# Kernel tuning notes

Measured on AMD Instinct MI355X. Metric: run time of the kernel, lower is better.

The kernel has to match this reference:

```python
import jax, jax.numpy as jnp
import numpy as np

N_HEADS = 16
DIM = 1024
HW = 32
B = 8


def _conv3x3(x, W, b):
    # x: [B, C, H, W], W: [O, I, 3, 3] (OIHW), padding 1 == SAME for stride 1
    y = jax.lax.conv_general_dilated(
        x, W, window_strides=(1, 1), padding='SAME',
        dimension_numbers=('NCHW', 'OIHW', 'NCHW'))
    return y + b[None, :, None, None]


def setup_inputs() -> dict:
    key = jax.random.key(0)
    ks = jax.random.split(key, 8)
    f32 = jnp.float32
    q = jax.random.normal(ks[0], (B, DIM, HW, HW), f32)
    k = jax.random.normal(ks[1], (B, DIM, HW, HW), f32)
    v = jax.random.normal(ks[2], (B, DIM, HW, HW), f32)
    Wq = jax.random.normal(ks[3], (DIM, DIM, 3, 3), f32) * 0.02
    Wk = jax.random.normal(ks[4], (DIM, DIM, 3, 3), f32) * 0.02
    Wv = jax.random.normal(ks[5], (DIM, DIM, 3, 3), f32) * 0.02
    Wo = jax.random.normal(ks[6], (DIM, DIM), f32) * 0.02
    bq = jnp.zeros((DIM,), f32); bk = jnp.zeros((DIM,), f32)
    bv = jnp.zeros((DIM,), f32); bo = jnp.zeros((DIM,), f32)
    mask = jax.random.randint(ks[7], (B, DIM, DIM), 0, 2, jnp.int32)
    return {'q': q, 'k': k, 'v': v, 'Wq': Wq, 'bq': bq, 'Wk': Wk, 'bk': bk,
            'Wv': Wv, 'bv': bv, 'Wo': Wo, 'bo': bo, 'mask': mask}


def reference(q, k, v, Wq, bq, Wk, bk, Wv, bv, Wo, bo, mask):
    Bq, C, H, W = q.shape  # C == dim, tokens = channels
    h = N_HEADS
    d = (H * W) // h  # head dim

    def split_heads(x):
        # [B, C, H, W] -> [B, h, C, d]
        return x.reshape(Bq, C, h, d).transpose(0, 2, 1, 3)

    qh = split_heads(_conv3x3(q, Wq, bq))
    kh = split_heads(_conv3x3(k, Wk, bk))
    vh = split_heads(_conv3x3(v, Wv, bv))

    scale = 1.0 / np.sqrt(d).astype(np.float32)
    attn = jnp.einsum('bhtd,bhsd->bhts', qh, kh) * scale  # [B, h, C, C]
    attn = jnp.where(mask[:, None, :, :] == 0, jnp.float32(-1e9), attn)
    w = jax.nn.softmax(attn, axis=-1)  # attn_dropout rate = 0 -> identity
    out = jnp.einsum('bhts,bhsd->bhtd', w, vh)  # [B, h, C, d]
    out = out.transpose(0, 2, 1, 3).reshape(Bq, C, h * d)  # [B, C, H*W]
    out = out @ Wo.T + bo  # Linear(dim, dim); H*W == dim
    return out
```

## Files before the change

### kernel.cpp

```cpp
#include <hip/hip_runtime.h>

typedef __attribute__((ext_vector_type(8))) short bh8;
typedef __attribute__((ext_vector_type(4))) short bh4;
typedef __attribute__((ext_vector_type(4))) float f32x4;

__device__ __forceinline__ short f2bf(float f) {
  union { float f; unsigned u; } a; a.f = f;
  unsigned r = a.u + 0x7FFFu + ((a.u >> 16) & 1u);
  return (short)(r >> 16);
}

__device__ __forceinline__ void g2l16(const short* g, short* l) {
  __builtin_amdgcn_global_load_lds(
      (const __attribute__((address_space(1))) void*)g,
      (__attribute__((address_space(3))) void*)l, 16, 0, 0);
}

__device__ __forceinline__ void barrier_raw() {
  asm volatile("" ::: "memory");
  __builtin_amdgcn_s_barrier();
  asm volatile("" ::: "memory");
}

__global__ __launch_bounds__(256) void zero_halo(short* __restrict__ xP) {
  int z = blockIdx.y;
  short* base = xP + (size_t)z * 1183744;
  int ri = blockIdx.x * 2 + (threadIdx.x >> 7);
  int row;
  if (ri < 34) row = ri;
  else if (ri < 68) row = 1122 + (ri - 34);
  else { int j = ri - 68; int y = (j >> 1) + 1; int x = (j & 1) ? 33 : 0; row = y * 34 + x; }
  int col = (threadIdx.x & 127) * 8;
  bh8 zv = {0, 0, 0, 0, 0, 0, 0, 0};
  *(bh8*)(base + (size_t)row * 1024 + col) = zv;
}

__global__ __launch_bounds__(256) void transpose3(
    const float* __restrict__ q, const float* __restrict__ k, const float* __restrict__ v,
    short* __restrict__ qP, short* __restrict__ kP, short* __restrict__ vP) {
  int z = blockIdx.z; int tensor = z >> 3, b = z & 7;
  const float* src = tensor == 0 ? q : (tensor == 1 ? k : v);
  short* dst = tensor == 0 ? qP : (tensor == 1 ? kP : vP);
  src += (size_t)b * 1048576; dst += (size_t)b * 1183744;
  int row0 = blockIdx.y * 64;
  int col0 = blockIdx.x * 64;
  __shared__ short t[64][72];
  int tid = threadIdx.x;
#pragma unroll
  for (int i = 0; i < 2; ++i) {
    int cid = tid + i * 256;
    int r = cid >> 3, co = (cid & 7) * 8;
    const float* p = src + (size_t)(row0 + r) * 1024 + col0 + co;
    float4 f0 = *(const float4*)(p);
    float4 f1 = *(const float4*)(p + 4);
    t[co + 0][r] = f2bf(f0.x); t[co + 1][r] = f2bf(f0.y);
    t[co + 2][r] = f2bf(f0.z); t[co + 3][r] = f2bf(f0.w);
    t[co + 4][r] = f2bf(f1.x); t[co + 5][r] = f2bf(f1.y);
    t[co + 6][r] = f2bf(f1.z); t[co + 7][r] = f2bf(f1.w);
  }
  __syncthreads();
#pragma unroll
  for (int i = 0; i < 2; ++i) {
    int cid = tid + i * 256;
    int sr = cid >> 3, cc = (cid & 7) * 8;
    bh8 val = *(const bh8*)&t[sr][cc];
    int tok = col0 + sr;
    int pr = ((tok >> 5) + 1) * 34 + (tok & 31) + 1;
    *(bh8*)(dst + (size_t)pr * 1024 + row0 + cc) = val;
  }
}

__global__ __launch_bounds__(256) void wperm3(
    const float* __restrict__ Wq, const float* __restrict__ Wk, const float* __restrict__ Wv,
    short* __restrict__ WpQ, short* __restrict__ WpK, short* __restrict__ WpV) {
  int z = blockIdx.y;
  const float* W = z == 0 ? Wq : (z == 1 ? Wk : Wv);
  short* Wp = z == 0 ? WpQ : (z == 1 ? WpK : WpV);
  int idx = blockIdx.x * 256 + threadIdx.x;
  const float* wsrc = W + (size_t)idx * 9;
#pragma unroll
  for (int t = 0; t < 9; ++t) Wp[(size_t)t * 1048576 + idx] = f2bf(wsrc[t]);
}

__global__ __launch_bounds__(256) void cvt_bf(const float* __restrict__ src,
                                              short* __restrict__ dst) {
  int idx = (blockIdx.x * 256 + threadIdx.x) * 4;
  float4 f = *(const float4*)(src + idx);
  bh4 o; o[0] = f2bf(f.x); o[1] = f2bf(f.y); o[2] = f2bf(f.z); o[3] = f2bf(f.w);
  *(bh4*)(dst + idx) = o;
}

__global__ __launch_bounds__(256) void mask_pack(const int* __restrict__ m,
                                                 unsigned* __restrict__ mp) {
  int idx = blockIdx.x * 256 + threadIdx.x;
  const int* src = m + (size_t)idx * 32;
  unsigned wv = 0;
#pragma unroll
  for (int j = 0; j < 32; j += 4) {
    int4 a = *(const int4*)(src + j);
    wv |= ((unsigned)(a.x & 1) << j) | ((unsigned)(a.y & 1) << (j + 1)) |
          ((unsigned)(a.z & 1) << (j + 2)) | ((unsigned)(a.w & 1) << (j + 3));
  }
  mp[idx] = wv;
}

__global__ __launch_bounds__(256, 2) void conv_gemm_td(
    const short* __restrict__ WpQ, const short* __restrict__ WpK, const short* __restrict__ WpV,
    const short* __restrict__ xPq, const short* __restrict__ xPk, const short* __restrict__ xPv,
    short* __restrict__ cQ, short* __restrict__ cK, short* __restrict__ cVT,
    const float* __restrict__ bq, const float* __restrict__ bk, const float* __restrict__ bv,
    int convSel) {
  __shared__ short lds[36864];
  int tid = threadIdx.x, lane = tid & 63, wid = tid >> 6;

  int fid = blockIdx.x + (blockIdx.y << 2) + ((int)blockIdx.z << 5);
  int nwg = (int)gridDim.z << 5;
  int cpx = nwg >> 3;
  int swz = (fid & 7) * cpx + (fid >> 3);
  int mtile = swz & 3, ntile = (swz >> 2) & 7, z = swz >> 5;

  int conv = convSel >= 0 ? convSel : (z >> 3);
  int b = convSel >= 0 ? z : (z & 7);
  const short* Wp = conv == 0 ? WpQ : (conv == 1 ? WpK : WpV);
  const short* xP = conv == 0 ? xPq : (conv == 1 ? xPk : xPv);
  short* out = conv == 0 ? cQ : (conv == 1 ? cK : cVT);
  const float* bias = conv == 0 ? bq : (conv == 1 ? bk : bv);
  int XisA = (conv == 2);
  int mbase = mtile * 256, nbase = ntile * 128;
  const short* xb = xP + (size_t)b * 1183744;

  int srow = tid >> 2;
  int lsl = (tid & 3) ^ ((tid >> 3) & 3);
  int gcol = lsl * 8;
  const short* pA0; const short* pB0;
  ptrdiff_t jA, jB;
  if (!XisA) {
    pA0 = Wp + (size_t)(mbase + srow) * 1024 + gcol;
    jA = 65536;
    int tok = nbase + srow;
    pB0 = xb + (size_t)(((tok >> 5) + 1) * 34 + (tok & 31) + 1) * 1024 + gcol;
    jB = 69632;
  } else {
    int ta = mbase + srow;
    pA0 = xb + (size_t)(((ta >> 5) + 1) * 34 + (ta & 31) + 1) * 1024 + gcol;
    jA = 69632;
    pB0 = Wp + (size_t)(nbase + srow) * 1024 + gcol;
    jB = 65536;
  }
  int sdst = tid * 8;

  int pslot = (((lane >> 4) ^ ((lane >> 1) & 3)) << 3);
  int wr = wid >> 1, wc = wid & 1;
  int rdA = (wr * 128 + (lane & 15)) * 32 + pslot;
  int rdB = 8192 + (wc * 64 + (lane & 15)) * 32 + pslot;

  f32x4 acc[8][4] = {};

#define STAGE(U, SRB) do { \
    int u_ = (U); \
    int tap_ = u_ >> 5, kk_ = (u_ & 31) << 5; \
    int ty_ = (tap_ * 11) >> 5; \
    ptrdiff_t dW_ = (ptrdiff_t)tap_ * 1048576 + kk_; \
    ptrdiff_t dX_ = (ptrdiff_t)(ty_ * 34 + (tap_ - ty_ * 3) - 35) * 1024 + kk_; \
    ptrdiff_t dA_ = XisA ? dX_ : dW_, dB_ = XisA ? dW_ : dX_; \
    short* du_ = &lds[(SRB) + sdst]; \
    g2l16(pA0 + dA_,          du_); \
    g2l16(pA0 + dA_ + jA,     du_ + 2048); \
    g2l16(pA0 + dA_ + 2 * jA, du_ + 4096); \
    g2l16(pA0 + dA_ + 3 * jA, du_ + 6144); \
    g2l16(pB0 + dB_,          du_ + 8192); \
    g2l16(pB0 + dB_ + jB,     du_ + 10240); \
  } while (0)

  STAGE(0, 0);
  STAGE(1, 12288);
  asm volatile("s_waitcnt vmcnt(6)" ::: "memory");
  barrier_raw();

#define TILEBODY(RB, T, DOSTAGE, SRB, WSTR) do { \
    const short* Lp = &lds[(RB)]; \
    bh8 afr[4], bfr[4], afr2[4]; \
    _Pragma("unroll") for (int nt = 0; nt < 4; ++nt) \
      bfr[nt] = *(const bh8*)(Lp + rdB + nt * 512); \
    _Pragma("unroll") for (int mt = 0; mt < 4; ++mt) \
      afr[mt] = *(const bh8*)(Lp + rdA + mt * 512); \
    if (DOSTAGE) STAGE((T) + 2, SRB); \
    __builtin_amdgcn_s_setprio(1); \
    _Pragma("unroll") for (int mt = 0; mt < 4; ++mt) { \
      _Pragma("unroll") for (int nt = 0; nt < 4; ++nt) \
        acc[mt][nt] = __builtin_amdgcn_mfma_f32_16x16x32_bf16( \
            afr[mt], bfr[nt], acc[mt][nt], 0, 0, 0); \
    } \
    __builtin_amdgcn_s_setprio(0); \
    _Pragma("unroll") for (int mt = 0; mt < 4; ++mt) \
      afr2[mt] = *(const bh8*)(Lp + rdA + 2048 + mt * 512); \
    __builtin_amdgcn_s_setprio(1); \
    _Pragma("unroll") for (int mt = 0; mt < 4; ++mt) { \
      _Pragma("unroll") for (int nt = 0; nt < 4; ++nt) \
        acc[4 + mt][nt] = __builtin_amdgcn_mfma_f32_16x16x32_bf16( \
            afr2[mt], bfr[nt], acc[4 + mt][nt], 0, 0, 0); \
    } \
    __builtin_amdgcn_s_setprio(0); \
    asm volatile(WSTR ::: "memory"); \
    barrier_raw(); \
  } while (0)

#pragma unroll 1
  for (int it = 0; it < 95; ++it) {
    int t0 = it * 3;
    TILEBODY(0,     t0 + 0, true, 24576, "s_waitcnt vmcnt(6)");
    TILEBODY(12288, t0 + 1, true, 0,     "s_waitcnt vmcnt(6)");
    TILEBODY(24576, t0 + 2, true, 12288, "s_waitcnt vmcnt(6)");
  }
  TILEBODY(0,     285, true,  24576, "s_waitcnt vmcnt(6)");
  TILEBODY(12288, 286, false, 0,     "s_waitcnt vmcnt(0)");
  TILEBODY(24576, 287, false, 0,     "");

#undef TILEBODY
#undef STAGE

  size_t ob = (size_t)b * 1048576;
#pragma unroll
  for (int mt = 0; mt < 8; ++mt) {
#pragma unroll
    for (int nt = 0; nt < 4; ++nt) {
      int m0 = mbase + wr * 128 + mt * 16 + ((lane >> 4) << 2);
      int nn = nbase + wc * 64 + nt * 16 + (lane & 15);
#pragma unroll
      for (int r = 0; r < 4; ++r) {
        float bvv = bias[XisA ? nn : (m0 + r)];
        out[ob + (size_t)(m0 + r) * 1024 + nn] = f2bf(acc[mt][nt][r] + bvv);
      }
    }
  }
}

__global__ __launch_bounds__(256) void attn(
    const short* __restrict__ Qc, const short* __restrict__ Kc,
    const short* __restrict__ VT, const unsigned* __restrict__ Mp,
    short* __restrict__ AO) {
  __shared__ short sQ[64][72];
  __shared__ short sK[128][72];
  __shared__ short sV[64][136];
  __shared__ short sP[64][136];
  int tid = threadIdx.x, lane = tid & 63, w = tid >> 6;
  int qbase = blockIdx.x * 64, h = blockIdx.y, b = blockIdx.z;
  int j0 = h * 64;
  const short* Qb = Qc + (size_t)b * 1048576;
  const short* Kb = Kc + (size_t)b * 1048576;
  const short* Vb = VT + (size_t)b * 1048576;
  const unsigned* Mpb = Mp + (size_t)b * 32768;
  const float scale = 0.125f;

#pragma unroll
  for (int i = 0; i < 2; ++i) {
    int cid = tid + i * 256;
    int row = cid >> 3, co = (cid & 7) * 8;
    *(bh8*)&sQ[row][co] = *(const bh8*)(Qb + (size_t)(qbase + row) * 1024 + j0 + co);
  }
  __syncthreads();

  int tg = qbase + w * 16 + (lane & 15);
  int rsel = ((lane >> 4) << 2);
  float mrow = -3.0e38f, lrow = 0.0f;
  f32x4 oacc[4] = {};

  for (int st = 0; st < 8; ++st) {
#pragma unroll
    for (int i = 0; i < 4; ++i) {
      int cid = tid + i * 256;
      int row = cid >> 3, co = (cid & 7) * 8;
      *(bh8*)&sK[row][co] = *(const bh8*)(Kb + (size_t)(st * 128 + row) * 1024 + j0 + co);
      int vrow = cid >> 4, vco = (cid & 15) * 8;
      *(bh8*)&sV[vrow][vco] = *(const bh8*)(Vb + (size_t)(j0 + vrow) * 1024 + st * 128 + vco);
    }
    __syncthreads();

    f32x4 sacc[8];
#pragma unroll
    for (int mt = 0; mt < 8; ++mt) {
      f32x4 a = {0.f, 0.f, 0.f, 0.f};
      bh8 kf = *(const bh8*)&sK[mt * 16 + (lane & 15)][(lane >> 4) * 8];
      bh8 qf = *(const bh8*)&sQ[w * 16 + (lane & 15)][(lane >> 4) * 8];
      a = __builtin_amdgcn_mfma_f32_16x16x32_bf16(kf, qf, a, 0, 0, 0);
      kf = *(const bh8*)&sK[mt * 16 + (lane & 15)][32 + (lane >> 4) * 8];
      qf = *(const bh8*)&sQ[w * 16 + (lane & 15)][32 + (lane >> 4) * 8];
      a = __builtin_amdgcn_mfma_f32_16x16x32_bf16(kf, qf, a, 0, 0, 0);
      sacc[mt] = a;
    }

    uint4 Mw = *(const uint4*)(Mpb + (size_t)tg * 32 + st * 4);
    float tmax = -3.0e38f;
#pragma unroll
    for (int mt = 0; mt < 8; ++mt) {
      unsigned mwv = ((const unsigned*)&Mw)[mt >> 1] >> ((mt & 1) * 16 + rsel);
      f32x4 vv;
      vv[0] = (mwv & 1u) ? sacc[mt][0] * scale : -1e9f;
      vv[1] = (mwv & 2u) ? sacc[mt][1] * scale : -1e9f;
      vv[2] = (mwv & 4u) ? sacc[mt][2] * scale : -1e9f;
      vv[3] = (mwv & 8u) ? sacc[mt][3] * scale : -1e9f;
      sacc[mt] = vv;
      tmax = fmaxf(tmax, fmaxf(fmaxf(vv[0], vv[1]), fmaxf(vv[2], vv[3])));
    }
    tmax = fmaxf(tmax, __shfl_xor(tmax, 16, 64));
    tmax = fmaxf(tmax, __shfl_xor(tmax, 32, 64));
    float mnew = fmaxf(mrow, tmax);
    float alpha = __expf(fminf(mrow - mnew, 0.f));

    float sum = 0.f;
    uint4 Mw2 = Mw;
#pragma unroll
    for (int mt = 0; mt < 8; ++mt) {
      unsigned mwv = ((const unsigned*)&Mw2)[mt >> 1] >> ((mt & 1) * 16 + rsel);
      float p0 = (mwv & 1u) ? __expf(fminf(sacc[mt][0] - mnew, 0.f)) : 0.f;
      float p1 = (mwv & 2u) ? __expf(fminf(sacc[mt][1] - mnew, 0.f)) : 0.f;
      float p2 = (mwv & 4u) ? __expf(fminf(sacc[mt][2] - mnew, 0.f)) : 0.f;
      float p3 = (mwv & 8u) ? __expf(fminf(sacc[mt][3] - mnew, 0.f)) : 0.f;
      sum += (p0 + p1) + (p2 + p3);
      bh4 p; p[0] = f2bf(p0); p[1] = f2bf(p1); p[2] = f2bf(p2); p[3] = f2bf(p3);
      *(bh4*)&sP[w * 16 + (lane & 15)][mt * 16 + rsel] = p;
    }
    sum += __shfl_xor(sum, 16, 64);
    sum += __shfl_xor(sum, 32, 64);
    lrow = lrow * alpha + sum;
    mrow = mnew;

    float al[4];
#pragma unroll
    for (int r = 0; r < 4; ++r) al[r] = __shfl(alpha, rsel + r, 64);
#pragma unroll
    for (int nt = 0; nt < 4; ++nt)
#pragma unroll
      for (int r = 0; r < 4; ++r) oacc[nt][r] *= al[r];
    __syncthreads();

#pragma unroll
    for (int k0 = 0; k0 < 4; ++k0) {
      bh8 pf = *(const bh8*)&sP[w * 16 + (lane & 15)][k0 * 32 + (lane >> 4) * 8];
#pragma unroll
      for (int nt = 0; nt < 4; ++nt) {
        bh8 vf = *(const bh8*)&sV[nt * 16 + (lane & 15)][k0 * 32 + (lane >> 4) * 8];
        oacc[nt] = __builtin_amdgcn_mfma_f32_16x16x32_bf16(pf, vf, oacc[nt], 0, 0, 0);
      }
    }
    __syncthreads();
  }

  float rl[4];
#pragma unroll
  for (int r = 0; r < 4; ++r) rl[r] = 1.0f / __shfl(lrow, rsel + r, 64);
  size_t ob = (size_t)b * 1048576;
#pragma unroll
  for (int nt = 0; nt < 4; ++nt) {
    int j = nt * 16 + (lane & 15);
    int t0 = qbase + w * 16 + rsel;
#pragma unroll
    for (int r = 0; r < 4; ++r)
      AO[ob + (size_t)(t0 + r) * 1024 + j0 + j] = f2bf(oacc[nt][r] * rl[r]);
  }
}

__global__ __launch_bounds__(256) void gemm_bt(
    const short* __restrict__ A, const short* __restrict__ Bm,
    float* __restrict__ out, const float* __restrict__ bias) {
  __shared__ short sA[4096];
  __shared__ short sB[4096];
  int tid = threadIdx.x, lane = tid & 63, w = tid >> 6;
  int mbase = blockIdx.x * 128, nbase = blockIdx.y * 128;
  int colsh = (lane & 3) * 8;
  int ldsoff[2]; const short* ap[2]; const short* bp[2];
#pragma unroll
  for (int i = 0; i < 2; ++i) {
    int row = 32 * w + 16 * i + (lane >> 2);
    ldsoff[i] = (2 * w + i) * 512 + lane * 8;
    ap[i] = A + (size_t)(mbase + row) * 1024 + colsh;
    bp[i] = Bm + (size_t)(nbase + row) * 1024 + colsh;
  }
  f32x4 acc[4][4] = {};
  int wm = (w >> 1) * 64, wn = (w & 1) * 64;
  for (int kt = 0; kt < 1024; kt += 32) {
#pragma unroll
    for (int i = 0; i < 2; ++i) {
      g2l16(ap[i] + kt, sA + ldsoff[i]);
      g2l16(bp[i] + kt, sB + ldsoff[i]);
    }
    __syncthreads();
    bh8 af[4], bfr[4];
#pragma unroll
    for (int mt = 0; mt < 4; ++mt)
      af[mt] = *(const bh8*)&sA[(wm + mt * 16 + (lane & 15)) * 32 + (lane >> 4) * 8];
#pragma unroll
    for (int nt = 0; nt < 4; ++nt)
      bfr[nt] = *(const bh8*)&sB[(wn + nt * 16 + (lane & 15)) * 32 + (lane >> 4) * 8];
#pragma unroll
    for (int mt = 0; mt < 4; ++mt)
#pragma unroll
      for (int nt = 0; nt < 4; ++nt)
        acc[mt][nt] = __builtin_amdgcn_mfma_f32_16x16x32_bf16(af[mt], bfr[nt], acc[mt][nt], 0, 0, 0);
    __syncthreads();
  }
#pragma unroll
  for (int mt = 0; mt < 4; ++mt) {
#pragma unroll
    for (int nt = 0; nt < 4; ++nt) {
      int m0 = mbase + wm + mt * 16 + ((lane >> 4) << 2);
      int n = nbase + wn + nt * 16 + (lane & 15);
      float bv = bias[n];
#pragma unroll
      for (int r = 0; r < 4; ++r)
        out[(size_t)(m0 + r) * 1024 + n] = acc[mt][nt][r] + bv;
    }
  }
}

extern "C" void kernel_launch(void* const* d_in, const int* in_sizes, int n_in,
                              void* d_out, int out_size, void* d_ws, size_t ws_size,
                              hipStream_t stream) {
  (void)in_sizes; (void)n_in; (void)out_size;
  const float* q    = (const float*)d_in[0];
  const float* k    = (const float*)d_in[1];
  const float* v    = (const float*)d_in[2];
  const float* Wq   = (const float*)d_in[3];
  const float* bq   = (const float*)d_in[4];
  const float* Wk   = (const float*)d_in[5];
  const float* bk   = (const float*)d_in[6];
  const float* Wv   = (const float*)d_in[7];
  const float* bv   = (const float*)d_in[8];
  const float* Wo   = (const float*)d_in[9];
  const float* bo   = (const float*)d_in[10];
  const int*   mask = (const int*)d_in[11];
  float* out = (float*)d_out;
  char* ws = (char*)d_ws;

  const size_t XPE = 1156ull * 1024 * 8;
  const size_t XPB = XPE * 2;
  const size_t WPE = 9ull * 1048576;
  short* xPq = (short*)ws;
  short* xPk = xPq + XPE;
  short* xPv = xPk + XPE;
  short* WpQ = (short*)(ws + 3 * XPB);
  short* WpK = WpQ + WPE;
  short* WpV = WpK + WPE;
  char* p2 = ws + 3 * XPB + 3 * WPE * 2;

  bool fused = ws_size >= 167000000ull;
  short *cQ, *cK, *cVT, *WoB, *AO; unsigned* Mpk;
  if (fused) {
    cQ  = (short*)(p2);
    cK  = (short*)(p2 + 16777216);
    cVT = (short*)(p2 + 33554432);
    WoB = (short*)(p2 + 50331648);
    Mpk = (unsigned*)(p2 + 52428800);
    AO  = xPq;
  } else {
    cQ  = (short*)(p2);
    WoB = (short*)(p2 + 16777216);
    Mpk = (unsigned*)(p2 + 18874368);
    cK  = xPq;
    cVT = xPk;
    AO  = xPv;
  }

  zero_halo<<<dim3(66, 24), dim3(256), 0, stream>>>(xPq);
  transpose3<<<dim3(16, 16, 24), dim3(256), 0, stream>>>(q, k, v, xPq, xPk, xPv);
  wperm3<<<dim3(4096, 3), dim3(256), 0, stream>>>(Wq, Wk, Wv, WpQ, WpK, WpV);
  cvt_bf<<<dim3(1024), dim3(256), 0, stream>>>(Wo, WoB);
  mask_pack<<<dim3(1024), dim3(256), 0, stream>>>(mask, Mpk);
  if (fused) {
    conv_gemm_td<<<dim3(4, 8, 24), dim3(256), 0, stream>>>(
        WpQ, WpK, WpV, xPq, xPk, xPv, cQ, cK, cVT, bq, bk, bv, -1);
  } else {
    conv_gemm_td<<<dim3(4, 8, 8), dim3(256), 0, stream>>>(
        WpQ, WpK, WpV, xPq, xPk, xPv, cQ, cK, cVT, bq, bk, bv, 0);
    conv_gemm_td<<<dim3(4, 8, 8), dim3(256), 0, stream>>>(
        WpQ, WpK, WpV, xPq, xPk, xPv, cQ, cK, cVT, bq, bk, bv, 1);
    conv_gemm_td<<<dim3(4, 8, 8), dim3(256), 0, stream>>>(
        WpQ, WpK, WpV, xPq, xPk, xPv, cQ, cK, cVT, bq, bk, bv, 2);
  }
  attn<<<dim3(16, 16, 8), dim3(256), 0, stream>>>(cQ, cK, cVT, Mpk, AO);
  gemm_bt<<<dim3(64, 8), dim3(256), 0, stream>>>(AO, WoB, out, bo);
}
```

Measured before the change: 802.7 us.

## Double-buffer MFMA register fragments and deepen LDS prefetch to three stages

```diff
diff --git a/kernel.cpp b/kernel.cpp
--- a/kernel.cpp
+++ b/kernel.cpp
@@ -155,6 +155,7 @@
   int rdB = 8192 + (wc * 64 + (lane & 15)) * 32 + pslot;
 
   f32x4 acc[8][4] = {};
+  bh8 aX[8], bX[4], aY[8], bY[4];
 
 #define STAGE(U, SRB) do { \
     int u_ = (U); \
@@ -172,51 +173,59 @@
     g2l16(pB0 + dB_ + jB,     du_ + 10240); \
   } while (0)
 
-  STAGE(0, 0);
-  STAGE(1, 12288);
-  asm volatile("s_waitcnt vmcnt(6)" ::: "memory");
-  barrier_raw();
-
-#define TILEBODY(RB, T, DOSTAGE, SRB, WSTR) do { \
-    const short* Lp = &lds[(RB)]; \
-    bh8 afr[4], bfr[4], afr2[4]; \
+#define LOADF(AF, BF, RB) do { \
+    const short* Ln_ = &lds[(RB)]; \
     _Pragma("unroll") for (int nt = 0; nt < 4; ++nt) \
-      bfr[nt] = *(const bh8*)(Lp + rdB + nt * 512); \
-    _Pragma("unroll") for (int mt = 0; mt < 4; ++mt) \
-      afr[mt] = *(const bh8*)(Lp + rdA + mt * 512); \
-    if (DOSTAGE) STAGE((T) + 2, SRB); \
+      BF[nt] = *(const bh8*)(Ln_ + rdB + nt * 512); \
+    _Pragma("unroll") for (int mt = 0; mt < 8; ++mt) \
+      AF[mt] = *(const bh8*)(Ln_ + rdA + (mt & 3) * 512 + (mt >> 2) * 2048); \
+  } while (0)
+
+#define MFMA32(AF, BF) do { \
     __builtin_amdgcn_s_setprio(1); \
-    _Pragma("unroll") for (int mt = 0; mt < 4; ++mt) { \
+    _Pragma("unroll") for (int mt = 0; mt < 8; ++mt) { \
       _Pragma("unroll") for (int nt = 0; nt < 4; ++nt) \
         acc[mt][nt] = __builtin_amdgcn_mfma_f32_16x16x32_bf16( \
-            afr[mt], bfr[nt], acc[mt][nt], 0, 0, 0); \
+            AF[mt], BF[nt], acc[mt][nt], 0, 0, 0); \
     } \
     __builtin_amdgcn_s_setprio(0); \
-    _Pragma("unroll") for (int mt = 0; mt < 4; ++mt) \
-      afr2[mt] = *(const bh8*)(Lp + rdA + 2048 + mt * 512); \
-    __builtin_amdgcn_s_setprio(1); \
-    _Pragma("unroll") for (int mt = 0; mt < 4; ++mt) { \
-      _Pragma("unroll") for (int nt = 0; nt < 4; ++nt) \
-        acc[4 + mt][nt] = __builtin_amdgcn_mfma_f32_16x16x32_bf16( \
-            afr2[mt], bfr[nt], acc[4 + mt][nt], 0, 0, 0); \
-    } \
-    __builtin_amdgcn_s_setprio(0); \
+  } while (0)
+
+#define TILEBODY(RN, T, AFc, BFc, AFn, BFn, DOSTAGE, SRB, WSTR) do { \
+    LOADF(AFn, BFn, RN); \
+    if (DOSTAGE) STAGE((T) + 3, SRB); \
+    MFMA32(AFc, BFc); \
     asm volatile(WSTR ::: "memory"); \
     barrier_raw(); \
   } while (0)
 
+  STAGE(0, 0);
+  STAGE(1, 12288);
+  STAGE(2, 24576);
+  asm volatile("s_waitcnt vmcnt(6)" ::: "memory");
+  barrier_raw();
+  LOADF(aX, bX, 0);
+
 #pragma unroll 1
-  for (int it = 0; it < 95; ++it) {
-    int t0 = it * 3;
-    TILEBODY(0,     t0 + 0, true, 24576, "s_waitcnt vmcnt(6)");
-    TILEBODY(12288, t0 + 1, true, 0,     "s_waitcnt vmcnt(6)");
-    TILEBODY(24576, t0 + 2, true, 12288, "s_waitcnt vmcnt(6)");
-  }
-  TILEBODY(0,     285, true,  24576, "s_waitcnt vmcnt(6)");
-  TILEBODY(12288, 286, false, 0,     "s_waitcnt vmcnt(0)");
-  TILEBODY(24576, 287, false, 0,     "");
+  for (int it = 0; it < 47; ++it) {
+    int t0 = it * 6;
+    TILEBODY(12288, t0 + 0, aX, bX, aY, bY, true, 0,     "s_waitcnt vmcnt(6)");
+    TILEBODY(24576, t0 + 1, aY, bY, aX, bX, true, 12288, "s_waitcnt vmcnt(6)");
+    TILEBODY(0,     t0 + 2, aX, bX, aY, bY, true, 24576, "s_waitcnt vmcnt(6)");
+    TILEBODY(12288, t0 + 3, aY, bY, aX, bX, true, 0,     "s_waitcnt vmcnt(6)");
+    TILEBODY(24576, t0 + 4, aX, bX, aY, bY, true, 12288, "s_waitcnt vmcnt(6)");
+    TILEBODY(0,     t0 + 5, aY, bY, aX, bX, true, 24576, "s_waitcnt vmcnt(6)");
+  }
+  TILEBODY(12288, 282, aX, bX, aY, bY, true,  0,     "s_waitcnt vmcnt(6)");
+  TILEBODY(24576, 283, aY, bY, aX, bX, true,  12288, "s_waitcnt vmcnt(6)");
+  TILEBODY(0,     284, aX, bX, aY, bY, true,  24576, "s_waitcnt vmcnt(6)");
+  TILEBODY(12288, 285, aY, bY, aX, bX, false, 0,     "s_waitcnt vmcnt(0)");
+  TILEBODY(24576, 286, aX, bX, aY, bY, false, 0,     "");
+  MFMA32(aY, bY);
 
 #undef TILEBODY
+#undef MFMA32
+#undef LOADF
 #undef STAGE
 
   size_t ob = (size_t)b * 1048576;
```

Measured after the change: 808.8 us. No clear change (+0.8%).
